# Kernel tuning notes

Measured on AMD Instinct MI355X. Metric: run time of the kernel, lower is better.

## Reference

```python
import jax, jax.numpy as jnp
import numpy as np

UNITS = 1024
INPUT_DIM = 512
BATCH = 2048

def setup_inputs() -> dict:
    key = jax.random.key(0)
    k1, k2, k3, k4 = jax.random.split(key, 4)
    return {
        "inputs": jax.random.normal(k1, (BATCH, INPUT_DIM), dtype=jnp.float32),
        "h_tm1": jax.random.normal(k2, (BATCH, UNITS), dtype=jnp.float32),
        "c_tm1": jax.random.normal(k3, (BATCH, UNITS), dtype=jnp.float32),
        # keras 'random_normal' initializer: stddev 0.05
        "kernel": jax.random.normal(k4, (UNITS + INPUT_DIM, 4 * UNITS), dtype=jnp.float32) * 0.05,
    }

def reference(inputs, h_tm1, c_tm1, kernel):
    # z = concat([h, x]) @ kernel ; kernel rows: [units (h-block); input_dim (x-block)]
    z = jnp.concatenate([h_tm1, inputs], axis=-1) @ kernel  # [B, 4*units]
    z0, z1, z2, z3 = jnp.split(z, 4, axis=-1)
    i = jax.nn.sigmoid(z0)
    f = jax.nn.sigmoid(z1)
    c_tilde = jnp.tanh(z2)
    o = jax.nn.sigmoid(z3)
    c = f * c_tm1 + i * c_tilde
    h = o * jnp.tanh(c)
    return (h, c)
```

## Files before the change

### kernel.cpp

```cpp
#include <hip/hip_runtime.h>
#include <hip/hip_bf16.h>
#include <stdint.h>

#define UNITS 1024
#define IDIM  512
#define BATCH 2048
#define KTOT  1536
#define NGATE 4096

#define BM 128
#define BU 32
#define BK 64

typedef short bf16x8 __attribute__((ext_vector_type(8)));
typedef float f32x4  __attribute__((ext_vector_type(4)));

#define AS3(p) ((__attribute__((address_space(3))) void*)(p))
#define AS1(p) ((const __attribute__((address_space(1))) void*)(p))

struct alignas(8) bh4 { __hip_bfloat16 a, b, c, d; };

__global__ __launch_bounds__(256) void cast_concat_a(
    const float* __restrict__ x, const float* __restrict__ h,
    __hip_bfloat16* __restrict__ A) {
  int tid = blockIdx.x * 256 + threadIdx.x;
  int r  = tid / (KTOT / 4);
  int c4 = tid % (KTOT / 4);
  int k  = c4 * 4;
  const float* src = (k < UNITS) ? (h + (size_t)r * UNITS + k)
                                 : (x + (size_t)r * IDIM + (k - UNITS));
  float4 v = *(const float4*)src;
  bh4 o = { __float2bfloat16(v.x), __float2bfloat16(v.y),
            __float2bfloat16(v.z), __float2bfloat16(v.w) };
  *(bh4*)(A + (size_t)r * KTOT + k) = o;
}

__global__ __launch_bounds__(256) void transpose_w(
    const float* __restrict__ W, __hip_bfloat16* __restrict__ Wt) {
  __shared__ float tile[32][33];
  int n0 = blockIdx.x * 32;
  int k0 = blockIdx.y * 32;
  int tx = threadIdx.x & 31;
  int ty = threadIdx.x >> 5;
#pragma unroll
  for (int r = 0; r < 32; r += 8)
    tile[ty + r][tx] = W[(size_t)(k0 + ty + r) * NGATE + n0 + tx];
  __syncthreads();
#pragma unroll
  for (int r = 0; r < 32; r += 8)
    Wt[(size_t)(n0 + ty + r) * KTOT + k0 + tx] = __float2bfloat16(tile[tx][ty + r]);
}

__global__ __launch_bounds__(256) void lstm_gemm(
    const __hip_bfloat16* __restrict__ A,
    const __hip_bfloat16* __restrict__ Wt,
    const float* __restrict__ c_tm1,
    float* __restrict__ out) {
  __shared__ __attribute__((aligned(128))) char ldsc[2 * 128 * BK * 2];

  const int tid  = threadIdx.x;
  const int w    = tid >> 6;
  const int lane = tid & 63;
  const int quad = lane >> 4;
  const int m16  = lane & 15;

  const int mb = blockIdx.x >> 5;
  const int ub = blockIdx.x & 31;
  const int m0 = mb * BM;
  const int u0 = ub * BU;

  f32x4 acc[2][8];
#pragma unroll
  for (int i = 0; i < 2; ++i)
#pragma unroll
    for (int j = 0; j < 8; ++j) {
      f32x4 z = {0.f, 0.f, 0.f, 0.f};
      acc[i][j] = z;
    }

  for (int kt = 0; kt < KTOT; kt += BK) {
#pragma unroll
    for (int s = 0; s < 8; ++s) {
      const int q     = s * 4 + w;
      const int rbase = (q & 15) * 8;
      const int lr    = rbase + (lane >> 3);
      const int k8    = (lane & 7) ^ (lr & 7);
      const __hip_bfloat16* src;
      if (q < 16) {
        src = A + (size_t)(m0 + lr) * KTOT + kt + k8 * 8;
      } else {
        const int row = ((lr >> 5) * UNITS) + u0 + (lr & 31);
        src = Wt + (size_t)row * KTOT + kt + k8 * 8;
      }
      char* dst = ldsc + (q < 16 ? 0 : 16384) + rbase * 128;
      __builtin_amdgcn_global_load_lds(AS1(src), AS3(dst), 16, 0, 0);
    }
    __syncthreads();

#pragma unroll
    for (int t = 0; t < 2; ++t) {
      bf16x8 a[2], b[8];
#pragma unroll
      for (int i = 0; i < 2; ++i) {
        const int row   = 32 * w + 16 * i + m16;
        const int k8    = t * 4 + quad;
        const int chunk = row * 8 + (k8 ^ (row & 7));
        a[i] = *(const bf16x8*)(ldsc + chunk * 16);
      }
#pragma unroll
      for (int j = 0; j < 8; ++j) {
        const int row   = 16 * j + m16;
        const int k8    = t * 4 + quad;
        const int chunk = row * 8 + (k8 ^ (row & 7));
        b[j] = *(const bf16x8*)(ldsc + 16384 + chunk * 16);
      }
#pragma unroll
      for (int j = 0; j < 8; ++j)
#pragma unroll
        for (int i = 0; i < 2; ++i)
          acc[i][j] = __builtin_amdgcn_mfma_f32_16x16x32_bf16(a[i], b[j], acc[i][j], 0, 0, 0);
    }
    __syncthreads();
  }

#pragma unroll
  for (int i = 0; i < 2; ++i)
#pragma unroll
    for (int uh = 0; uh < 2; ++uh)
#pragma unroll
      for (int reg = 0; reg < 4; ++reg) {
        const int r = m0 + 32 * w + 16 * i + quad * 4 + reg;
        const int u = u0 + uh * 16 + m16;
        const float z0 = acc[i][0 + uh][reg];
        const float z1 = acc[i][2 + uh][reg];
        const float z2 = acc[i][4 + uh][reg];
        const float z3 = acc[i][6 + uh][reg];
        const float ig = 1.f / (1.f + __expf(-z0));
        const float fg = 1.f / (1.f + __expf(-z1));
        const float ct = 1.f - 2.f / (__expf(2.f * z2) + 1.f);
        const float og = 1.f / (1.f + __expf(-z3));
        const float cc = fg * c_tm1[(size_t)r * UNITS + u] + ig * ct;
        const float hh = og * (1.f - 2.f / (__expf(2.f * cc) + 1.f));
        out[(size_t)r * UNITS + u] = hh;
        out[(size_t)BATCH * UNITS + (size_t)r * UNITS + u] = cc;
      }
}

__global__ __launch_bounds__(256) void lstm_naive(
    const float* __restrict__ x, const float* __restrict__ h,
    const float* __restrict__ c_tm1, const float* __restrict__ W,
    float* __restrict__ out) {
  int idx = blockIdx.x * 256 + threadIdx.x;
  int r = idx / UNITS;
  int u = idx % UNITS;
  float z[4] = {0.f, 0.f, 0.f, 0.f};
  for (int k = 0; k < KTOT; ++k) {
    float a = (k < UNITS) ? h[(size_t)r * UNITS + k] : x[(size_t)r * IDIM + k - UNITS];
#pragma unroll
    for (int g = 0; g < 4; ++g)
      z[g] += a * W[(size_t)k * NGATE + g * UNITS + u];
  }
  float ig = 1.f / (1.f + __expf(-z[0]));
  float fg = 1.f / (1.f + __expf(-z[1]));
  float ct = 1.f - 2.f / (__expf(2.f * z[2]) + 1.f);
  float og = 1.f / (1.f + __expf(-z[3]));
  float cc = fg * c_tm1[(size_t)r * UNITS + u] + ig * ct;
  float hh = og * (1.f - 2.f / (__expf(2.f * cc) + 1.f));
  out[(size_t)r * UNITS + u] = hh;
  out[(size_t)BATCH * UNITS + (size_t)r * UNITS + u] = cc;
}

extern "C" void kernel_launch(void* const* d_in, const int* in_sizes, int n_in,
                              void* d_out, int out_size, void* d_ws, size_t ws_size,
                              hipStream_t stream) {
  const float* x = (const float*)d_in[0];
  const float* h = (const float*)d_in[1];
  const float* c = (const float*)d_in[2];
  const float* W = (const float*)d_in[3];
  float* out = (float*)d_out;

  const size_t needA  = (size_t)BATCH * KTOT * sizeof(__hip_bfloat16);
  const size_t needWt = (size_t)NGATE * KTOT * sizeof(__hip_bfloat16);
  if (ws_size < needA + needWt) {
    hipLaunchKernelGGL(lstm_naive, dim3((BATCH * UNITS) / 256), dim3(256), 0, stream,
                       x, h, c, W, out);
    return;
  }

  __hip_bfloat16* A  = (__hip_bfloat16*)d_ws;
  __hip_bfloat16* Wt = (__hip_bfloat16*)((char*)d_ws + needA);

  hipLaunchKernelGGL(cast_concat_a, dim3((BATCH * (KTOT / 4)) / 256), dim3(256), 0,
                     stream, x, h, A);
  hipLaunchKernelGGL(transpose_w, dim3(NGATE / 32, KTOT / 32), dim3(256), 0,
                     stream, W, Wt);
  hipLaunchKernelGGL(lstm_gemm, dim3((BATCH / BM) * (UNITS / BU)), dim3(256), 0,
                     stream, A, Wt, c, out);
}
```

Baseline: 130.6 us.

## Fuse prep kernels, shrink GEMM tile to 64x32 and swizzle block order

After: 126.1 us. 3.4% less time.

```diff
diff --git a/kernel.cpp b/kernel.cpp
--- a/kernel.cpp
+++ b/kernel.cpp
@@ -7,10 +7,7 @@
 #define BATCH 2048
 #define KTOT  1536
 #define NGATE 4096
-
-#define BM 128
-#define BU 32
-#define BK 64
+#define BK    64
 
 typedef short bf16x8 __attribute__((ext_vector_type(8)));
 typedef float f32x4  __attribute__((ext_vector_type(4)));
@@ -18,132 +15,156 @@
 #define AS3(p) ((__attribute__((address_space(3))) void*)(p))
 #define AS1(p) ((const __attribute__((address_space(1))) void*)(p))
 
-struct alignas(8) bh4 { __hip_bfloat16 a, b, c, d; };
-
-__global__ __launch_bounds__(256) void cast_concat_a(
+union P8 { bf16x8 v; __hip_bfloat16 e[8]; };
+
+#define NBLK_A 1536
+#define NBLK_T 3072
+
+__global__ __launch_bounds__(256) void prep(
     const float* __restrict__ x, const float* __restrict__ h,
-    __hip_bfloat16* __restrict__ A) {
-  int tid = blockIdx.x * 256 + threadIdx.x;
-  int r  = tid / (KTOT / 4);
-  int c4 = tid % (KTOT / 4);
-  int k  = c4 * 4;
-  const float* src = (k < UNITS) ? (h + (size_t)r * UNITS + k)
-                                 : (x + (size_t)r * IDIM + (k - UNITS));
-  float4 v = *(const float4*)src;
-  bh4 o = { __float2bfloat16(v.x), __float2bfloat16(v.y),
-            __float2bfloat16(v.z), __float2bfloat16(v.w) };
-  *(bh4*)(A + (size_t)r * KTOT + k) = o;
-}
-
-__global__ __launch_bounds__(256) void transpose_w(
-    const float* __restrict__ W, __hip_bfloat16* __restrict__ Wt) {
-  __shared__ float tile[32][33];
-  int n0 = blockIdx.x * 32;
-  int k0 = blockIdx.y * 32;
-  int tx = threadIdx.x & 31;
-  int ty = threadIdx.x >> 5;
-#pragma unroll
-  for (int r = 0; r < 32; r += 8)
-    tile[ty + r][tx] = W[(size_t)(k0 + ty + r) * NGATE + n0 + tx];
-  __syncthreads();
-#pragma unroll
-  for (int r = 0; r < 32; r += 8)
-    Wt[(size_t)(n0 + ty + r) * KTOT + k0 + tx] = __float2bfloat16(tile[tx][ty + r]);
-}
-
-__global__ __launch_bounds__(256) void lstm_gemm(
+    const float* __restrict__ W,
+    __hip_bfloat16* __restrict__ A, __hip_bfloat16* __restrict__ Wt) {
+  __shared__ float tile[32][65];
+  const int tid = threadIdx.x;
+  if (blockIdx.x < NBLK_A) {
+    const int id = blockIdx.x * 256 + tid;
+    const int r = id / (KTOT / 8);
+    const int k = (id % (KTOT / 8)) * 8;
+    const float* src = (k < UNITS) ? h + (size_t)r * UNITS + k
+                                   : x + (size_t)r * IDIM + (k - UNITS);
+    const float4 v0 = ((const float4*)src)[0];
+    const float4 v1 = ((const float4*)src)[1];
+    P8 o;
+    o.e[0] = __float2bfloat16(v0.x); o.e[1] = __float2bfloat16(v0.y);
+    o.e[2] = __float2bfloat16(v0.z); o.e[3] = __float2bfloat16(v0.w);
+    o.e[4] = __float2bfloat16(v1.x); o.e[5] = __float2bfloat16(v1.y);
+    o.e[6] = __float2bfloat16(v1.z); o.e[7] = __float2bfloat16(v1.w);
+    *(bf16x8*)(A + (size_t)r * KTOT + k) = o.v;
+  } else {
+    const int b  = blockIdx.x - NBLK_A;
+    const int kb = b >> 7;
+    const int nb = b & 127;
+    const int k0 = kb * 64, n0 = nb * 32;
+    const int n4 = (tid & 7) * 4;
+    const int kk = tid >> 3;
+#pragma unroll
+    for (int rr = 0; rr < 64; rr += 32) {
+      const float4 v = *(const float4*)(W + (size_t)(k0 + kk + rr) * NGATE + n0 + n4);
+      tile[n4 + 0][kk + rr] = v.x; tile[n4 + 1][kk + rr] = v.y;
+      tile[n4 + 2][kk + rr] = v.z; tile[n4 + 3][kk + rr] = v.w;
+    }
+    __syncthreads();
+    const int n  = tid >> 3;
+    const int k8 = (tid & 7) * 8;
+    P8 o;
+#pragma unroll
+    for (int j = 0; j < 8; ++j) o.e[j] = __float2bfloat16(tile[n][k8 + j]);
+    *(bf16x8*)(Wt + (size_t)(n0 + n) * KTOT + k0 + k8) = o.v;
+  }
+}
+
+__global__ __launch_bounds__(256, 4) void lstm_gemm(
     const __hip_bfloat16* __restrict__ A,
     const __hip_bfloat16* __restrict__ Wt,
     const float* __restrict__ c_tm1,
     float* __restrict__ out) {
-  __shared__ __attribute__((aligned(128))) char ldsc[2 * 128 * BK * 2];
+  __shared__ __attribute__((aligned(128))) char lds[24576];
 
   const int tid  = threadIdx.x;
   const int w    = tid >> 6;
   const int lane = tid & 63;
   const int quad = lane >> 4;
   const int m16  = lane & 15;
-
-  const int mb = blockIdx.x >> 5;
-  const int ub = blockIdx.x & 31;
-  const int m0 = mb * BM;
-  const int u0 = ub * BU;
-
-  f32x4 acc[2][8];
+  const int wr   = w >> 1;
+  const int wc   = w & 1;
+
+  const int bi = blockIdx.x;
+  const int ub = ((bi & 7) << 2) | ((bi >> 3) & 3);
+  const int mb = bi >> 5;
+  const int m0 = mb * 64;
+  const int u0 = ub * 32;
+
+  const __hip_bfloat16* ptr[6];
+  int dstoff[6];
+#pragma unroll
+  for (int s = 0; s < 6; ++s) {
+    const int q = s * 4 + w;
+    if (q < 8) {
+      const int ci  = q * 64 + lane;
+      const int row = ci >> 3;
+      const int k8  = (ci & 7) ^ (row & 7);
+      ptr[s]    = A + (size_t)(m0 + row) * KTOT + k8 * 8;
+      dstoff[s] = q * 1024;
+    } else {
+      const int ci   = (q - 8) * 64 + lane;
+      const int vr   = ci >> 3;
+      const int k8   = (ci & 7) ^ (vr & 7);
+      const int wrow = ((vr >> 5) << 10) + u0 + (vr & 31);
+      ptr[s]    = Wt + (size_t)wrow * KTOT + k8 * 8;
+      dstoff[s] = 8192 + (q - 8) * 1024;
+    }
+  }
+
+  f32x4 acc[2][4];
 #pragma unroll
   for (int i = 0; i < 2; ++i)
 #pragma unroll
-    for (int j = 0; j < 8; ++j) {
+    for (int g = 0; g < 4; ++g) {
       f32x4 z = {0.f, 0.f, 0.f, 0.f};
-      acc[i][j] = z;
+      acc[i][g] = z;
     }
 
   for (int kt = 0; kt < KTOT; kt += BK) {
 #pragma unroll
-    for (int s = 0; s < 8; ++s) {
-      const int q     = s * 4 + w;
-      const int rbase = (q & 15) * 8;
-      const int lr    = rbase + (lane >> 3);
-      const int k8    = (lane & 7) ^ (lr & 7);
-      const __hip_bfloat16* src;
-      if (q < 16) {
-        src = A + (size_t)(m0 + lr) * KTOT + kt + k8 * 8;
-      } else {
-        const int row = ((lr >> 5) * UNITS) + u0 + (lr & 31);
-        src = Wt + (size_t)row * KTOT + kt + k8 * 8;
+    for (int s = 0; s < 6; ++s) {
+      __builtin_amdgcn_global_load_lds(AS1(ptr[s]), AS3(lds + dstoff[s]), 16, 0, 0);
+      ptr[s] += BK;
+    }
+    __syncthreads();
+
+#pragma unroll
+    for (int t = 0; t < 2; ++t) {
+      bf16x8 a[2], b[4];
+#pragma unroll
+      for (int i = 0; i < 2; ++i) {
+        const int row  = 32 * wr + 16 * i + m16;
+        const int slot = (t * 4 + quad) ^ (row & 7);
+        a[i] = *(const bf16x8*)(lds + (row * 8 + slot) * 16);
       }
-      char* dst = ldsc + (q < 16 ? 0 : 16384) + rbase * 128;
-      __builtin_amdgcn_global_load_lds(AS1(src), AS3(dst), 16, 0, 0);
+#pragma unroll
+      for (int g = 0; g < 4; ++g) {
+        const int vr   = g * 32 + wc * 16 + m16;
+        const int slot = (t * 4 + quad) ^ (vr & 7);
+        b[g] = *(const bf16x8*)(lds + 8192 + (vr * 8 + slot) * 16);
+      }
+#pragma unroll
+      for (int g = 0; g < 4; ++g)
+#pragma unroll
+        for (int i = 0; i < 2; ++i)
+          acc[i][g] = __builtin_amdgcn_mfma_f32_16x16x32_bf16(a[i], b[g], acc[i][g], 0, 0, 0);
     }
     __syncthreads();
-
-#pragma unroll
-    for (int t = 0; t < 2; ++t) {
-      bf16x8 a[2], b[8];
-#pragma unroll
-      for (int i = 0; i < 2; ++i) {
-        const int row   = 32 * w + 16 * i + m16;
-        const int k8    = t * 4 + quad;
-        const int chunk = row * 8 + (k8 ^ (row & 7));
-        a[i] = *(const bf16x8*)(ldsc + chunk * 16);
-      }
-#pragma unroll
-      for (int j = 0; j < 8; ++j) {
-        const int row   = 16 * j + m16;
-        const int k8    = t * 4 + quad;
-        const int chunk = row * 8 + (k8 ^ (row & 7));
-        b[j] = *(const bf16x8*)(ldsc + 16384 + chunk * 16);
-      }
-#pragma unroll
-      for (int j = 0; j < 8; ++j)
-#pragma unroll
-        for (int i = 0; i < 2; ++i)
-          acc[i][j] = __builtin_amdgcn_mfma_f32_16x16x32_bf16(a[i], b[j], acc[i][j], 0, 0, 0);
-    }
-    __syncthreads();
   }
 
 #pragma unroll
   for (int i = 0; i < 2; ++i)
 #pragma unroll
-    for (int uh = 0; uh < 2; ++uh)
-#pragma unroll
-      for (int reg = 0; reg < 4; ++reg) {
-        const int r = m0 + 32 * w + 16 * i + quad * 4 + reg;
-        const int u = u0 + uh * 16 + m16;
-        const float z0 = acc[i][0 + uh][reg];
-        const float z1 = acc[i][2 + uh][reg];
-        const float z2 = acc[i][4 + uh][reg];
-        const float z3 = acc[i][6 + uh][reg];
-        const float ig = 1.f / (1.f + __expf(-z0));
-        const float fg = 1.f / (1.f + __expf(-z1));
-        const float ct = 1.f - 2.f / (__expf(2.f * z2) + 1.f);
-        const float og = 1.f / (1.f + __expf(-z3));
-        const float cc = fg * c_tm1[(size_t)r * UNITS + u] + ig * ct;
-        const float hh = og * (1.f - 2.f / (__expf(2.f * cc) + 1.f));
-        out[(size_t)r * UNITS + u] = hh;
-        out[(size_t)BATCH * UNITS + (size_t)r * UNITS + u] = cc;
-      }
+    for (int reg = 0; reg < 4; ++reg) {
+      const int r = m0 + 32 * wr + 16 * i + quad * 4 + reg;
+      const int u = u0 + wc * 16 + m16;
+      const float z0 = acc[i][0][reg];
+      const float z1 = acc[i][1][reg];
+      const float z2 = acc[i][2][reg];
+      const float z3 = acc[i][3][reg];
+      const float ig = 1.f / (1.f + __expf(-z0));
+      const float fg = 1.f / (1.f + __expf(-z1));
+      const float ct = 1.f - 2.f / (__expf(2.f * z2) + 1.f);
+      const float og = 1.f / (1.f + __expf(-z3));
+      const float cc = fg * c_tm1[(size_t)r * UNITS + u] + ig * ct;
+      const float hh = og * (1.f - 2.f / (__expf(2.f * cc) + 1.f));
+      out[(size_t)r * UNITS + u] = hh;
+      out[(size_t)BATCH * UNITS + (size_t)r * UNITS + u] = cc;
+    }
 }
 
 __global__ __launch_bounds__(256) void lstm_naive(
@@ -190,10 +211,6 @@
   __hip_bfloat16* A  = (__hip_bfloat16*)d_ws;
   __hip_bfloat16* Wt = (__hip_bfloat16*)((char*)d_ws + needA);
 
-  hipLaunchKernelGGL(cast_concat_a, dim3((BATCH * (KTOT / 4)) / 256), dim3(256), 0,
-                     stream, x, h, A);
-  hipLaunchKernelGGL(transpose_w, dim3(NGATE / 32, KTOT / 32), dim3(256), 0,
-                     stream, W, Wt);
-  hipLaunchKernelGGL(lstm_gemm, dim3((BATCH / BM) * (UNITS / BU)), dim3(256), 0,
-                     stream, A, Wt, c, out);
-}
+  hipLaunchKernelGGL(prep, dim3(NBLK_A + NBLK_T), dim3(256), 0, stream, x, h, W, A, Wt);
+  hipLaunchKernelGGL(lstm_gemm, dim3(1024), dim3(256), 0, stream, A, Wt, c, out);
+}
```
